# Kernel tuning notes

Hardware: AMD Instinct MI355X
Metric: run time of the kernel (lower is better)

Reference implementation:

```python
import jax, jax.numpy as jnp
import numpy as np

N, G, C, A, E = 10000, 12, 64, 3, 50000
LN_EPS = 1e-5


def setup_inputs() -> dict:
    key = jax.random.key(0)
    ks = jax.random.split(key, 12)
    s = 0.05
    return {
        "x": jax.random.normal(ks[0], (N, G, C), jnp.float32),
        "edge_attr": jax.random.normal(ks[1], (E, G, G, A), jnp.float32),
        "W_kernel": jax.random.normal(ks[2], (A, C), jnp.float32) * s,   # depthwise kernel basis Linear(attr_dim->C)
        "conv_bias": jax.random.normal(ks[3], (C,), jnp.float32) * s,
        "ln_w": jnp.ones((C,), jnp.float32),
        "ln_b": jnp.zeros((C,), jnp.float32),
        "W1": jax.random.normal(ks[4], (C, C), jnp.float32) * s,          # stored [in,out]
        "b1": jax.random.normal(ks[5], (C,), jnp.float32) * s,
        "W2": jax.random.normal(ks[6], (C, C), jnp.float32) * s,
        "b2": jax.random.normal(ks[7], (C,), jnp.float32) * s,
        "layer_scale": jnp.full((1, C), 1e-6, jnp.float32),
        "edge_index": jax.random.randint(ks[8], (2, E), 0, N, jnp.int32),
        "batch": jnp.zeros((N,), jnp.int32),
    }


def reference(x, edge_attr, W_kernel, conv_bias, ln_w, ln_b, W1, b1, W2, b2,
              layer_scale, edge_index, batch):
    src, dst = edge_index[0], edge_index[1]
    x_j = x[src]                                            # [E,G,C] gather
    # depthwise fiber conv: m[e,g,c] = sum_{h,a} attr[e,g,h,a] * Wk[a,c] * x_j[e,h,c]
    # contract over source grid h first to avoid materializing the [E,G,G,C] kernel
    t = jnp.einsum('egha,ehc->egac', edge_attr, x_j)        # [E,G,A,C]
    m = jnp.einsum('egac,ac->egc', t, W_kernel)             # [E,G,C]
    agg = jnp.zeros_like(x).at[dst].add(m) + conv_bias      # scatter-add, [N,G,C]
    # LayerNorm over channel dim
    mu = jnp.mean(agg, axis=-1, keepdims=True)
    var = jnp.mean(jnp.square(agg - mu), axis=-1, keepdims=True)
    h = (agg - mu) * jax.lax.rsqrt(var + LN_EPS) * ln_w + ln_b
    # 2-layer MLP with exact GELU (torch default)
    h = jax.nn.gelu(h @ W1 + b1, approximate=False) @ W2 + b2
    h = layer_scale * h                                     # broadcast [1,C] over [N,G,C]
    return x + h                                            # residual (same shape)
```

## Files before the change

### kernel.cpp

```cpp
#include <hip/hip_runtime.h>
#include <math.h>

#define NN 10000
#define GG 12
#define CC 64
#define AA 3
#define EE 50000
#define LN_EPS 1e-5f
#define MAXDEG 64

typedef __attribute__((ext_vector_type(4))) float f4;
typedef __attribute__((ext_vector_type(4))) short s4;

union S4U { s4 s; unsigned int w[2]; };
union I2S { int i[2]; s4 s; };

__device__ __forceinline__ s4 pack4(float k0, float k1, float k2, float k3) {
    S4U t;
    t.w[0] = __builtin_amdgcn_perm(__float_as_uint(k1), __float_as_uint(k0), 0x07060302u);
    t.w[1] = __builtin_amdgcn_perm(__float_as_uint(k3), __float_as_uint(k2), 0x07060302u);
    return t.s;
}
__device__ __forceinline__ unsigned int pack2(float a, float b) {
    return __builtin_amdgcn_perm(__float_as_uint(b), __float_as_uint(a), 0x07060302u);
}

__device__ __forceinline__ f4 mfma_bf16(s4 a, s4 b, f4 c) {
#if __has_builtin(__builtin_amdgcn_mfma_f32_16x16x16bf16_1k)
    return __builtin_amdgcn_mfma_f32_16x16x16bf16_1k(a, b, c, 0, 0, 0);
#else
    asm volatile("v_mfma_f32_16x16x16_bf16 %0, %1, %2, %0" : "+v"(c) : "v"(a), "v"(b));
    return c;
#endif
}

__global__ __launch_bounds__(256) void xpack(const float* __restrict__ x,
                                             unsigned int* __restrict__ xp,
                                             int* __restrict__ cnt) {
    const int gid = blockIdx.x * 256 + threadIdx.x;
    if (gid < NN) cnt[gid] = 0;

    const int l  = threadIdx.x & 63;
    const int n  = blockIdx.x * 4 + (threadIdx.x >> 6);
    const int lm = l & 15;
    const int lg = l >> 4;

    unsigned int d[8];
    if (lg < 3) {
        const char* xb = (const char*)(x + n * (GG * CC)) + lg * 1024 + lm * 4;
#pragma unroll
        for (int t = 0; t < 4; ++t) {
            const float v0 = *(const float*)(xb + t * 64 + 0 * 256);
            const float v1 = *(const float*)(xb + t * 64 + 1 * 256);
            const float v2 = *(const float*)(xb + t * 64 + 2 * 256);
            const float v3 = *(const float*)(xb + t * 64 + 3 * 256);
            d[2 * t]     = pack2(v0, v1);
            d[2 * t + 1] = pack2(v2, v3);
        }
    } else {
#pragma unroll
        for (int k = 0; k < 8; ++k) d[k] = 0u;
    }
    unsigned int* o = xp + (size_t)n * 512 + l * 8;
    *(uint4*)o       = make_uint4(d[0], d[1], d[2], d[3]);
    *(uint4*)(o + 4) = make_uint4(d[4], d[5], d[6], d[7]);
}

__global__ __launch_bounds__(256) void bucket_fill(const int* __restrict__ ei,
                                                   int* __restrict__ cnt,
                                                   int* __restrict__ elist) {
    int e = blockIdx.x * 256 + threadIdx.x;
    if (e < EE) {
        int src = ei[e];
        int dst = ei[EE + e];
        int pos = atomicAdd(&cnt[dst], 1);
        if (pos < MAXDEG) elist[dst * MAXDEG + pos] = e | (src << 17);
    }
}

__global__ __launch_bounds__(512) void conv_mfma(
    const unsigned int* __restrict__ xp, const float* __restrict__ attr,
    const float* __restrict__ Wk,
    const int* __restrict__ cnt, const int* __restrict__ elist,
    float* __restrict__ agg) {
    __shared__ float lsa[8][2][432];

    const int l  = threadIdx.x & 63;
    const int w  = threadIdx.x >> 6;
    const int lm = l & 15;
    const int lg = l >> 4;

    const int fbase = (lm < 12 && lg < 3) ? (lm * 36 + lg * 12) : 0;
    const int a1l   = (l < 44) ? l : 43;

    float wk[3][4];
#pragma unroll
    for (int a = 0; a < 3; ++a)
#pragma unroll
        for (int t = 0; t < 4; ++t)
            wk[a][t] = Wk[a * CC + lm + 16 * t];

    for (int n = blockIdx.x * 8 + w; n < NN; n += gridDim.x * 8) {
        const int deg = min(cnt[n], MAXDEG);
        const int myE = elist[n * MAXDEG + l];

        f4 acc[3][4];
#pragma unroll
        for (int a = 0; a < 3; ++a)
#pragma unroll
            for (int t = 0; t < 4; ++t) acc[a][t] = (f4){0.f, 0.f, 0.f, 0.f};

        f4 Aa0, Aa1, Ab0, Ab1;
        int4 Xa0, Xa1, Xb0, Xb1;

#define LOADE(idx, A0, A1, X0, X1)                                              \
    {                                                                           \
        const int p = __builtin_amdgcn_readlane(myE, (idx));                    \
        const char* ab = (const char*)(attr + (size_t)(p & 0x1FFFF) * 432);     \
        A0 = *(const f4*)(ab + 16 * l);                                         \
        A1 = *(const f4*)(ab + 1024 + 16 * a1l);                                \
        const int* xb = (const int*)(xp + (size_t)(p >> 17) * 512 + 8 * l);     \
        X0 = *(const int4*)xb;                                                  \
        X1 = *(const int4*)(xb + 4);                                            \
    }

#define STAGE(slot, A0, A1)                                                     \
    {                                                                           \
        float* sw = &lsa[w][slot][0];                                           \
        *(f4*)(sw + 4 * l) = A0;                                                \
        if (l < 44) *(f4*)(sw + 256 + 4 * l) = A1;                              \
    }

#define COMPUTE(slot, X0, X1)                                                   \
    {                                                                           \
        I2S u0, u1, u2, u3;                                                     \
        u0.i[0] = X0.x; u0.i[1] = X0.y;                                         \
        u1.i[0] = X0.z; u1.i[1] = X0.w;                                         \
        u2.i[0] = X1.x; u2.i[1] = X1.y;                                         \
        u3.i[0] = X1.z; u3.i[1] = X1.w;                                         \
        const float* sr = &lsa[w][slot][0] + fbase;                             \
        const f4 q0 = *(const f4*)(sr);                                         \
        const f4 q1 = *(const f4*)(sr + 4);                                     \
        const f4 q2 = *(const f4*)(sr + 8);                                     \
        const s4 af0 = pack4(q0[0], q0[3], q1[2], q2[1]);                       \
        const s4 af1 = pack4(q0[1], q1[0], q1[3], q2[2]);                       \
        const s4 af2 = pack4(q0[2], q1[1], q2[0], q2[3]);                       \
        acc[0][0] = mfma_bf16(af0, u0.s, acc[0][0]);                            \
        acc[1][0] = mfma_bf16(af1, u0.s, acc[1][0]);                            \
        acc[2][0] = mfma_bf16(af2, u0.s, acc[2][0]);                            \
        acc[0][1] = mfma_bf16(af0, u1.s, acc[0][1]);                            \
        acc[1][1] = mfma_bf16(af1, u1.s, acc[1][1]);                            \
        acc[2][1] = mfma_bf16(af2, u1.s, acc[2][1]);                            \
        acc[0][2] = mfma_bf16(af0, u2.s, acc[0][2]);                            \
        acc[1][2] = mfma_bf16(af1, u2.s, acc[1][2]);                            \
        acc[2][2] = mfma_bf16(af2, u2.s, acc[2][2]);                            \
        acc[0][3] = mfma_bf16(af0, u3.s, acc[0][3]);                            \
        acc[1][3] = mfma_bf16(af1, u3.s, acc[1][3]);                            \
        acc[2][3] = mfma_bf16(af2, u3.s, acc[2][3]);                            \
    }

        if (deg > 0) LOADE(0, Aa0, Aa1, Xa0, Xa1);
        if (deg > 1) LOADE(1, Ab0, Ab1, Xb0, Xb1);
        if (deg > 0) STAGE(0, Aa0, Aa1);

        for (int j = 0; j < deg; j += 2) {
            COMPUTE(0, Xa0, Xa1);
            if (j + 2 < deg) LOADE(j + 2, Aa0, Aa1, Xa0, Xa1);
            if (j + 1 < deg) {
                STAGE(1, Ab0, Ab1);
                COMPUTE(1, Xb0, Xb1);
                if (j + 3 < deg) LOADE(j + 3, Ab0, Ab1, Xb0, Xb1);
                if (j + 2 < deg) STAGE(0, Aa0, Aa1);
            }
        }

#undef LOADE
#undef STAGE
#undef COMPUTE

        float* ob = agg + (size_t)n * (GG * CC);
        if (lg < 3) {
#pragma unroll
            for (int t = 0; t < 4; ++t) {
#pragma unroll
                for (int r = 0; r < 4; ++r) {
                    const float m = fmaf(acc[0][t][r], wk[0][t],
                                    fmaf(acc[1][t][r], wk[1][t],
                                         acc[2][t][r] * wk[2][t]));
                    ob[(lg * 4 + r) * CC + lm + 16 * t] = m;
                }
            }
        }
    }
}

__global__ __launch_bounds__(512) void ln_mlp_mfma(
    const float* __restrict__ x, const float* __restrict__ cb,
    const float* __restrict__ lnw, const float* __restrict__ lnb,
    const float* __restrict__ W1, const float* __restrict__ b1,
    const float* __restrict__ W2, const float* __restrict__ b2,
    const float* __restrict__ ls, float* __restrict__ out) {
    __shared__ float sbuf[8][16 * 68];

    const int l  = threadIdx.x & 63;
    const int wv = threadIdx.x >> 6;
    const int lm = l & 15;
    const int lg = l >> 4;
    const int f0 = (blockIdx.x * 8 + wv) * 16;
    if (f0 >= NN * GG) return;

    const float* aggp = out + (size_t)(f0 + lm) * CC + 4 * lg;
    f4 h4[4];
#pragma unroll
    for (int kt = 0; kt < 4; ++kt) h4[kt] = *(const f4*)(aggp + 16 * kt);

    f4 cb4[4], lw4[4], lb4[4];
#pragma unroll
    for (int kt = 0; kt < 4; ++kt) {
        cb4[kt] = *(const f4*)(cb  + 4 * lg + 16 * kt);
        lw4[kt] = *(const f4*)(lnw + 4 * lg + 16 * kt);
        lb4[kt] = *(const f4*)(lnb + 4 * lg + 16 * kt);
    }

    float s = 0.f, s2 = 0.f;
#pragma unroll
    for (int kt = 0; kt < 4; ++kt)
#pragma unroll
        for (int j = 0; j < 4; ++j) {
            const float v = h4[kt][j] + cb4[kt][j];
            h4[kt][j] = v;
            s += v; s2 += v * v;
        }
    s  += __shfl_xor(s, 16);  s  += __shfl_xor(s, 32);
    s2 += __shfl_xor(s2, 16); s2 += __shfl_xor(s2, 32);
    const float mu  = s * (1.f / 64.f);
    const float inv = rsqrtf(s2 * (1.f / 64.f) - mu * mu + LN_EPS);

    s4 hf[4];
#pragma unroll
    for (int kt = 0; kt < 4; ++kt) {
        const float n0 = (h4[kt][0] - mu) * inv * lw4[kt][0] + lb4[kt][0];
        const float n1 = (h4[kt][1] - mu) * inv * lw4[kt][1] + lb4[kt][1];
        const float n2 = (h4[kt][2] - mu) * inv * lw4[kt][2] + lb4[kt][2];
        const float n3 = (h4[kt][3] - mu) * inv * lw4[kt][3] + lb4[kt][3];
        hf[kt] = pack4(n0, n1, n2, n3);
    }

    s4 w1f[4][4];
#pragma unroll
    for (int mt = 0; mt < 4; ++mt)
#pragma unroll
        for (int kt = 0; kt < 4; ++kt) {
            const int kb = 4 * lg + 16 * kt;
            const int m  = lm + 16 * mt;
            w1f[mt][kt] = pack4(W1[(kb + 0) * CC + m], W1[(kb + 1) * CC + m],
                                W1[(kb + 2) * CC + m], W1[(kb + 3) * CC + m]);
        }

    f4 z[4];
#pragma unroll
    for (int mt = 0; mt < 4; ++mt) z[mt] = (f4){0.f, 0.f, 0.f, 0.f};
#pragma unroll
    for (int mt = 0; mt < 4; ++mt)
#pragma unroll
        for (int kt = 0; kt < 4; ++kt)
            z[mt] = mfma_bf16(w1f[mt][kt], hf[kt], z[mt]);

    s4 gf[4];
#pragma unroll
    for (int mt = 0; mt < 4; ++mt) {
        const f4 b14 = *(const f4*)(b1 + 16 * mt + 4 * lg);
        float g[4];
#pragma unroll
        for (int r = 0; r < 4; ++r) {
            const float zz = z[mt][r] + b14[r];
            g[r] = 0.5f * zz * (1.f + erff(zz * 0.70710678118654752f));
        }
        gf[mt] = pack4(g[0], g[1], g[2], g[3]);
    }

    s4 w2f[4][4];
#pragma unroll
    for (int mt = 0; mt < 4; ++mt)
#pragma unroll
        for (int kt = 0; kt < 4; ++kt) {
            const int kb = 4 * lg + 16 * kt;
            const int m  = lm + 16 * mt;
            w2f[mt][kt] = pack4(W2[(kb + 0) * CC + m], W2[(kb + 1) * CC + m],
                                W2[(kb + 2) * CC + m], W2[(kb + 3) * CC + m]);
        }

    f4 o[4];
#pragma unroll
    for (int mt = 0; mt < 4; ++mt) o[mt] = (f4){0.f, 0.f, 0.f, 0.f};
#pragma unroll
    for (int mt = 0; mt < 4; ++mt)
#pragma unroll
        for (int kt = 0; kt < 4; ++kt)
            o[mt] = mfma_bf16(w2f[mt][kt], gf[kt], o[mt]);

    float* sb = sbuf[wv];
    const int fbase = lm * 68;
    const int swz   = (l & 7) << 2;
#pragma unroll
    for (int mt = 0; mt < 4; ++mt)
#pragma unroll
        for (int r = 0; r < 4; ++r)
            sb[fbase + ((16 * mt + 4 * lg + r) ^ swz)] = o[mt][r];

    const f4 b2q = *(const f4*)(b2 + 4 * lm);
    const f4 lsq = *(const f4*)(ls + 4 * lm);

#pragma unroll
    for (int rr = 0; rr < 4; ++rr) {
        const int R   = rr * 4 + lg;
        const int col = 4 * lm;
        const f4 ov = *(const f4*)(&sb[R * 68 + (col ^ ((R & 7) << 2))]);
        const f4 xv = *(const f4*)(x + (size_t)(f0 + R) * CC + col);
        f4 res;
#pragma unroll
        for (int k = 0; k < 4; ++k)
            res[k] = fmaf(lsq[k], ov[k] + b2q[k], xv[k]);
        *(f4*)(out + (size_t)(f0 + R) * CC + col) = res;
    }
}

extern "C" void kernel_launch(void* const* d_in, const int* in_sizes, int n_in,
                              void* d_out, int out_size, void* d_ws, size_t ws_size,
                              hipStream_t stream) {
    const float* x    = (const float*)d_in[0];
    const float* attr = (const float*)d_in[1];
    const float* Wk   = (const float*)d_in[2];
    const float* cb   = (const float*)d_in[3];
    const float* lnw  = (const float*)d_in[4];
    const float* lnb  = (const float*)d_in[5];
    const float* W1   = (const float*)d_in[6];
    const float* b1   = (const float*)d_in[7];
    const float* W2   = (const float*)d_in[8];
    const float* b2   = (const float*)d_in[9];
    const float* ls   = (const float*)d_in[10];
    const int*   ei   = (const int*)d_in[11];
    float* out = (float*)d_out;

    int* cnt   = (int*)d_ws;
    int* elist = cnt + NN;
    unsigned int* xp = (unsigned int*)(elist + NN * MAXDEG);

    xpack<<<NN / 4, 256, 0, stream>>>(x, xp, cnt);
    bucket_fill<<<(EE + 255) / 256, 256, 0, stream>>>(ei, cnt, elist);
    conv_mfma<<<640, 512, 0, stream>>>(xp, attr, Wk, cnt, elist, out);
    ln_mlp_mfma<<<938, 512, 0, stream>>>(x, cb, lnw, lnb, W1, b1, W2, b2, ls, out);
}
```

Measured before the change: 76.63 us.

## Balance conv edge work across waves via per-block shared edge queue

Each block now handles 4 destination nodes and gathers all of their edges into a shared-memory queue. The 4 waves take edges round-robin, so imbalance from uneven node degree within a block is reduced. Each edge's MFMA result is projected by Wk and added atomically into per-node LDS accumulators, then written out together. In exchange it pays for LDS float atomics on every edge, extra block-wide barriers, and a launch of one block per 4 nodes instead of a persistent grid.

```diff
diff --git a/kernel.cpp b/kernel.cpp
--- a/kernel.cpp
+++ b/kernel.cpp
@@ -78,21 +78,47 @@
     }
 }
 
-__global__ __launch_bounds__(512) void conv_mfma(
+__global__ __launch_bounds__(256) void conv_mfma(
     const unsigned int* __restrict__ xp, const float* __restrict__ attr,
     const float* __restrict__ Wk,
     const int* __restrict__ cnt, const int* __restrict__ elist,
     float* __restrict__ agg) {
-    __shared__ float lsa[8][2][432];
+    __shared__ float lsa[4][2][432];
+    __shared__ float nacc[4][GG][68];
+    __shared__ int   qp_[4 * MAXDEG];
+    __shared__ int   qn_[4 * MAXDEG];
+    __shared__ int   degs[4];
 
     const int l  = threadIdx.x & 63;
     const int w  = threadIdx.x >> 6;
+    const int n  = blockIdx.x * 4 + w;
     const int lm = l & 15;
     const int lg = l >> 4;
 
     const int fbase = (lm < 12 && lg < 3) ? (lm * 36 + lg * 12) : 0;
     const int a1l   = (l < 44) ? l : 43;
 
+    const int deg = min(cnt[n], MAXDEG);
+    const int myE = elist[n * MAXDEG + l];
+    if (l == 0) degs[w] = deg;
+
+    {
+        float* nf = &nacc[0][0][0];
+        const f4 z4 = (f4){0.f, 0.f, 0.f, 0.f};
+        for (int q = threadIdx.x; q < 816; q += 256) *(f4*)(nf + q * 4) = z4;
+    }
+    __syncthreads();
+
+    int off = 0, total = 0;
+#pragma unroll
+    for (int j = 0; j < 4; ++j) {
+        const int d = degs[j];
+        if (j < w) off += d;
+        total += d;
+    }
+    if (l < deg) { qp_[off + l] = myE; qn_[off + l] = w; }
+    __syncthreads();
+
     float wk[3][4];
 #pragma unroll
     for (int a = 0; a < 3; ++a)
@@ -100,26 +126,21 @@
         for (int t = 0; t < 4; ++t)
             wk[a][t] = Wk[a * CC + lm + 16 * t];
 
-    for (int n = blockIdx.x * 8 + w; n < NN; n += gridDim.x * 8) {
-        const int deg = min(cnt[n], MAXDEG);
-        const int myE = elist[n * MAXDEG + l];
-
-        f4 acc[3][4];
-#pragma unroll
-        for (int a = 0; a < 3; ++a)
-#pragma unroll
-            for (int t = 0; t < 4; ++t) acc[a][t] = (f4){0.f, 0.f, 0.f, 0.f};
-
-        f4 Aa0, Aa1, Ab0, Ab1;
-        int4 Xa0, Xa1, Xb0, Xb1;
-
-#define LOADE(idx, A0, A1, X0, X1)                                              \
+    const int cntLoc = (total > w) ? ((total - w + 3) >> 2) : 0;
+
+    int Pa = 0, Sa = 0, Pb = 0, Sb = 0;
+    f4 Aa0, Aa1, Ab0, Ab1;
+    int4 Xa0, Xa1, Xb0, Xb1;
+
+#define QLOAD(k, P, S, A0, A1, X0, X1)                                          \
     {                                                                           \
-        const int p = __builtin_amdgcn_readlane(myE, (idx));                    \
-        const char* ab = (const char*)(attr + (size_t)(p & 0x1FFFF) * 432);     \
+        const int qi = w + 4 * (k);                                             \
+        P = __builtin_amdgcn_readfirstlane(qp_[qi]);                            \
+        S = __builtin_amdgcn_readfirstlane(qn_[qi]);                            \
+        const char* ab = (const char*)(attr + (size_t)(P & 0x1FFFF) * 432);     \
         A0 = *(const f4*)(ab + 16 * l);                                         \
         A1 = *(const f4*)(ab + 1024 + 16 * a1l);                                \
-        const int* xb = (const int*)(xp + (size_t)(p >> 17) * 512 + 8 * l);     \
+        const int* xb = (const int*)(xp + (size_t)(P >> 17) * 512 + 8 * l);     \
         X0 = *(const int4*)xb;                                                  \
         X1 = *(const int4*)(xb + 4);                                            \
     }
@@ -131,7 +152,7 @@
         if (l < 44) *(f4*)(sw + 256 + 4 * l) = A1;                              \
     }
 
-#define COMPUTE(slot, X0, X1)                                                   \
+#define COMPUTE(slot, S, X0, X1)                                                \
     {                                                                           \
         I2S u0, u1, u2, u3;                                                     \
         u0.i[0] = X0.x; u0.i[1] = X0.y;                                         \
@@ -145,52 +166,63 @@
         const s4 af0 = pack4(q0[0], q0[3], q1[2], q2[1]);                       \
         const s4 af1 = pack4(q0[1], q1[0], q1[3], q2[2]);                       \
         const s4 af2 = pack4(q0[2], q1[1], q2[0], q2[3]);                       \
-        acc[0][0] = mfma_bf16(af0, u0.s, acc[0][0]);                            \
-        acc[1][0] = mfma_bf16(af1, u0.s, acc[1][0]);                            \
-        acc[2][0] = mfma_bf16(af2, u0.s, acc[2][0]);                            \
-        acc[0][1] = mfma_bf16(af0, u1.s, acc[0][1]);                            \
-        acc[1][1] = mfma_bf16(af1, u1.s, acc[1][1]);                            \
-        acc[2][1] = mfma_bf16(af2, u1.s, acc[2][1]);                            \
-        acc[0][2] = mfma_bf16(af0, u2.s, acc[0][2]);                            \
-        acc[1][2] = mfma_bf16(af1, u2.s, acc[1][2]);                            \
-        acc[2][2] = mfma_bf16(af2, u2.s, acc[2][2]);                            \
-        acc[0][3] = mfma_bf16(af0, u3.s, acc[0][3]);                            \
-        acc[1][3] = mfma_bf16(af1, u3.s, acc[1][3]);                            \
-        acc[2][3] = mfma_bf16(af2, u3.s, acc[2][3]);                            \
-    }
-
-        if (deg > 0) LOADE(0, Aa0, Aa1, Xa0, Xa1);
-        if (deg > 1) LOADE(1, Ab0, Ab1, Xb0, Xb1);
-        if (deg > 0) STAGE(0, Aa0, Aa1);
-
-        for (int j = 0; j < deg; j += 2) {
-            COMPUTE(0, Xa0, Xa1);
-            if (j + 2 < deg) LOADE(j + 2, Aa0, Aa1, Xa0, Xa1);
-            if (j + 1 < deg) {
-                STAGE(1, Ab0, Ab1);
-                COMPUTE(1, Xb0, Xb1);
-                if (j + 3 < deg) LOADE(j + 3, Ab0, Ab1, Xb0, Xb1);
-                if (j + 2 < deg) STAGE(0, Aa0, Aa1);
-            }
-        }
-
-#undef LOADE
+        const f4 z4 = (f4){0.f, 0.f, 0.f, 0.f};                                 \
+        f4 acc[3][4];                                                           \
+        acc[0][0] = mfma_bf16(af0, u0.s, z4);                                   \
+        acc[1][0] = mfma_bf16(af1, u0.s, z4);                                   \
+        acc[2][0] = mfma_bf16(af2, u0.s, z4);                                   \
+        acc[0][1] = mfma_bf16(af0, u1.s, z4);                                   \
+        acc[1][1] = mfma_bf16(af1, u1.s, z4);                                   \
+        acc[2][1] = mfma_bf16(af2, u1.s, z4);                                   \
+        acc[0][2] = mfma_bf16(af0, u2.s, z4);                                   \
+        acc[1][2] = mfma_bf16(af1, u2.s, z4);                                   \
+        acc[2][2] = mfma_bf16(af2, u2.s, z4);                                   \
+        acc[0][3] = mfma_bf16(af0, u3.s, z4);                                   \
+        acc[1][3] = mfma_bf16(af1, u3.s, z4);                                   \
+        acc[2][3] = mfma_bf16(af2, u3.s, z4);                                   \
+        _Pragma("unroll")                                                       \
+        for (int t = 0; t < 4; ++t) {                                           \
+            _Pragma("unroll")                                                   \
+            for (int r = 0; r < 4; ++r) {                                       \
+                const float mv = fmaf(acc[0][t][r], wk[0][t],                   \
+                                 fmaf(acc[1][t][r], wk[1][t],                   \
+                                      acc[2][t][r] * wk[2][t]));                \
+                if (lg < 3)                                                     \
+                    atomicAdd(&nacc[S][lg * 4 + r][lm + 16 * t], mv);           \
+            }                                                                   \
+        }                                                                       \
+    }
+
+    if (cntLoc > 0) QLOAD(0, Pa, Sa, Aa0, Aa1, Xa0, Xa1);
+    if (cntLoc > 1) QLOAD(1, Pb, Sb, Ab0, Ab1, Xb0, Xb1);
+    if (cntLoc > 0) STAGE(0, Aa0, Aa1);
+
+    for (int k = 0; k < cntLoc; k += 2) {
+        COMPUTE(0, Sa, Xa0, Xa1);
+        if (k + 2 < cntLoc) QLOAD(k + 2, Pa, Sa, Aa0, Aa1, Xa0, Xa1);
+        if (k + 1 < cntLoc) {
+            STAGE(1, Ab0, Ab1);
+            COMPUTE(1, Sb, Xb0, Xb1);
+            if (k + 3 < cntLoc) QLOAD(k + 3, Pb, Sb, Ab0, Ab1, Xb0, Xb1);
+            if (k + 2 < cntLoc) STAGE(0, Aa0, Aa1);
+        }
+    }
+
+#undef QLOAD
 #undef STAGE
 #undef COMPUTE
 
-        float* ob = agg + (size_t)n * (GG * CC);
-        if (lg < 3) {
-#pragma unroll
-            for (int t = 0; t < 4; ++t) {
-#pragma unroll
-                for (int r = 0; r < 4; ++r) {
-                    const float m = fmaf(acc[0][t][r], wk[0][t],
-                                    fmaf(acc[1][t][r], wk[1][t],
-                                         acc[2][t][r] * wk[2][t]));
-                    ob[(lg * 4 + r) * CC + lm + 16 * t] = m;
-                }
-            }
-        }
+    __syncthreads();
+
+    float* ob = agg + (size_t)blockIdx.x * 4 * (GG * CC);
+#pragma unroll
+    for (int q = 0; q < 3; ++q) {
+        const int fi  = threadIdx.x + q * 256;
+        const int s   = fi / 192;
+        const int rem = fi % 192;
+        const int g   = rem / 16;
+        const int c4  = (rem % 16) * 4;
+        *(f4*)(ob + fi * 4) = *(const f4*)(&nacc[s][g][c4]);
     }
 }
 
@@ -348,6 +380,6 @@
 
     xpack<<<NN / 4, 256, 0, stream>>>(x, xp, cnt);
     bucket_fill<<<(EE + 255) / 256, 256, 0, stream>>>(ei, cnt, elist);
-    conv_mfma<<<640, 512, 0, stream>>>(xp, attr, Wk, cnt, elist, out);
+    conv_mfma<<<NN / 4, 256, 0, stream>>>(xp, attr, Wk, cnt, elist, out);
     ln_mlp_mfma<<<938, 512, 0, stream>>>(x, cb, lnw, lnb, W1, b1, W2, b2, ls, out);
 }
```

Result: slower. 268.1 us (+249.9%).

## Fuse depthwise conv aggregation with LayerNorm and MLP in one kernel

Applied to the files above, without the earlier changes.

Merges the conv gather-MFMA kernel and the LayerNorm+MLP kernel into one kernel where each wave owns a node and keeps its 12x64 aggregate in LDS instead of writing it to global memory and reading it back. The conv bias is folded in when the aggregate is formed, and the persistent grid-stride loop is replaced by one wave per node with a 4-wave block. This removes one launch and a global round trip of the aggregate, but the MLP now processes only 12 useful rows out of a 16-row MFMA tile (4 padded with zeros), and every wave reloads W1/W2 weights.

```diff
diff --git a/kernel.cpp b/kernel.cpp
--- a/kernel.cpp
+++ b/kernel.cpp
@@ -78,21 +78,29 @@
     }
 }
 
-__global__ __launch_bounds__(512) void conv_mfma(
+__global__ __launch_bounds__(256) void conv_fused(
     const unsigned int* __restrict__ xp, const float* __restrict__ attr,
-    const float* __restrict__ Wk,
-    const int* __restrict__ cnt, const int* __restrict__ elist,
-    float* __restrict__ agg) {
-    __shared__ float lsa[8][2][432];
+    const float* __restrict__ Wk,  const float* __restrict__ cb,
+    const float* __restrict__ lnw, const float* __restrict__ lnb,
+    const float* __restrict__ W1,  const float* __restrict__ b1,
+    const float* __restrict__ W2,  const float* __restrict__ b2,
+    const float* __restrict__ ls,  const float* __restrict__ x,
+    const int* __restrict__ cnt,   const int* __restrict__ elist,
+    float* __restrict__ out) {
+    __shared__ float scratch[4][1088];
 
     const int l  = threadIdx.x & 63;
     const int w  = threadIdx.x >> 6;
+    const int n  = blockIdx.x * 4 + w;
     const int lm = l & 15;
     const int lg = l >> 4;
 
     const int fbase = (lm < 12 && lg < 3) ? (lm * 36 + lg * 12) : 0;
     const int a1l   = (l < 44) ? l : 43;
 
+    const int deg = min(cnt[n], MAXDEG);
+    const int myE = elist[n * MAXDEG + l];
+
     float wk[3][4];
 #pragma unroll
     for (int a = 0; a < 3; ++a)
@@ -100,18 +108,14 @@
         for (int t = 0; t < 4; ++t)
             wk[a][t] = Wk[a * CC + lm + 16 * t];
 
-    for (int n = blockIdx.x * 8 + w; n < NN; n += gridDim.x * 8) {
-        const int deg = min(cnt[n], MAXDEG);
-        const int myE = elist[n * MAXDEG + l];
-
-        f4 acc[3][4];
-#pragma unroll
-        for (int a = 0; a < 3; ++a)
-#pragma unroll
-            for (int t = 0; t < 4; ++t) acc[a][t] = (f4){0.f, 0.f, 0.f, 0.f};
-
-        f4 Aa0, Aa1, Ab0, Ab1;
-        int4 Xa0, Xa1, Xb0, Xb1;
+    f4 acc[3][4];
+#pragma unroll
+    for (int a = 0; a < 3; ++a)
+#pragma unroll
+        for (int t = 0; t < 4; ++t) acc[a][t] = (f4){0.f, 0.f, 0.f, 0.f};
+
+    f4 Aa0, Aa1, Ab0, Ab1;
+    int4 Xa0, Xa1, Xb0, Xb1;
 
 #define LOADE(idx, A0, A1, X0, X1)                                              \
     {                                                                           \
@@ -126,7 +130,7 @@
 
 #define STAGE(slot, A0, A1)                                                     \
     {                                                                           \
-        float* sw = &lsa[w][slot][0];                                           \
+        float* sw = &scratch[w][(slot) * 432];                                  \
         *(f4*)(sw + 4 * l) = A0;                                                \
         if (l < 44) *(f4*)(sw + 256 + 4 * l) = A1;                              \
     }
@@ -138,7 +142,7 @@
         u1.i[0] = X0.z; u1.i[1] = X0.w;                                         \
         u2.i[0] = X1.x; u2.i[1] = X1.y;                                         \
         u3.i[0] = X1.z; u3.i[1] = X1.w;                                         \
-        const float* sr = &lsa[w][slot][0] + fbase;                             \
+        const float* sr = &scratch[w][(slot) * 432] + fbase;                    \
         const f4 q0 = *(const f4*)(sr);                                         \
         const f4 q1 = *(const f4*)(sr + 4);                                     \
         const f4 q2 = *(const f4*)(sr + 8);                                     \
@@ -159,65 +163,50 @@
         acc[2][3] = mfma_bf16(af2, u3.s, acc[2][3]);                            \
     }
 
-        if (deg > 0) LOADE(0, Aa0, Aa1, Xa0, Xa1);
-        if (deg > 1) LOADE(1, Ab0, Ab1, Xb0, Xb1);
-        if (deg > 0) STAGE(0, Aa0, Aa1);
-
-        for (int j = 0; j < deg; j += 2) {
-            COMPUTE(0, Xa0, Xa1);
-            if (j + 2 < deg) LOADE(j + 2, Aa0, Aa1, Xa0, Xa1);
-            if (j + 1 < deg) {
-                STAGE(1, Ab0, Ab1);
-                COMPUTE(1, Xb0, Xb1);
-                if (j + 3 < deg) LOADE(j + 3, Ab0, Ab1, Xb0, Xb1);
-                if (j + 2 < deg) STAGE(0, Aa0, Aa1);
-            }
-        }
+    if (deg > 0) LOADE(0, Aa0, Aa1, Xa0, Xa1);
+    if (deg > 1) LOADE(1, Ab0, Ab1, Xb0, Xb1);
+    if (deg > 0) STAGE(0, Aa0, Aa1);
+
+    for (int j = 0; j < deg; j += 2) {
+        COMPUTE(0, Xa0, Xa1);
+        if (j + 2 < deg) LOADE(j + 2, Aa0, Aa1, Xa0, Xa1);
+        if (j + 1 < deg) {
+            STAGE(1, Ab0, Ab1);
+            COMPUTE(1, Xb0, Xb1);
+            if (j + 3 < deg) LOADE(j + 3, Ab0, Ab1, Xb0, Xb1);
+            if (j + 2 < deg) STAGE(0, Aa0, Aa1);
+        }
+    }
 
 #undef LOADE
 #undef STAGE
 #undef COMPUTE
 
-        float* ob = agg + (size_t)n * (GG * CC);
-        if (lg < 3) {
-#pragma unroll
-            for (int t = 0; t < 4; ++t) {
-#pragma unroll
-                for (int r = 0; r < 4; ++r) {
-                    const float m = fmaf(acc[0][t][r], wk[0][t],
-                                    fmaf(acc[1][t][r], wk[1][t],
-                                         acc[2][t][r] * wk[2][t]));
-                    ob[(lg * 4 + r) * CC + lm + 16 * t] = m;
-                }
+    float* hb = &scratch[w][0];
+
+    if (lg < 3) {
+#pragma unroll
+        for (int t = 0; t < 4; ++t) {
+            const float cbT = cb[lm + 16 * t];
+#pragma unroll
+            for (int r = 0; r < 4; ++r) {
+                const float mv = fmaf(acc[0][t][r], wk[0][t],
+                                 fmaf(acc[1][t][r], wk[1][t],
+                                      acc[2][t][r] * wk[2][t])) + cbT;
+                hb[(4 * lg + r) * 68 + lm + 16 * t] = mv;
             }
         }
     }
-}
-
-__global__ __launch_bounds__(512) void ln_mlp_mfma(
-    const float* __restrict__ x, const float* __restrict__ cb,
-    const float* __restrict__ lnw, const float* __restrict__ lnb,
-    const float* __restrict__ W1, const float* __restrict__ b1,
-    const float* __restrict__ W2, const float* __restrict__ b2,
-    const float* __restrict__ ls, float* __restrict__ out) {
-    __shared__ float sbuf[8][16 * 68];
-
-    const int l  = threadIdx.x & 63;
-    const int wv = threadIdx.x >> 6;
-    const int lm = l & 15;
-    const int lg = l >> 4;
-    const int f0 = (blockIdx.x * 8 + wv) * 16;
-    if (f0 >= NN * GG) return;
-
-    const float* aggp = out + (size_t)(f0 + lm) * CC + 4 * lg;
+    *(f4*)(hb + (12 + lg) * 68 + 4 * lm) = (f4){0.f, 0.f, 0.f, 0.f};
+
     f4 h4[4];
 #pragma unroll
-    for (int kt = 0; kt < 4; ++kt) h4[kt] = *(const f4*)(aggp + 16 * kt);
-
-    f4 cb4[4], lw4[4], lb4[4];
+    for (int kt = 0; kt < 4; ++kt)
+        h4[kt] = *(const f4*)(hb + lm * 68 + 4 * lg + 16 * kt);
+
+    f4 lw4[4], lb4[4];
 #pragma unroll
     for (int kt = 0; kt < 4; ++kt) {
-        cb4[kt] = *(const f4*)(cb  + 4 * lg + 16 * kt);
         lw4[kt] = *(const f4*)(lnw + 4 * lg + 16 * kt);
         lb4[kt] = *(const f4*)(lnb + 4 * lg + 16 * kt);
     }
@@ -227,8 +216,7 @@
     for (int kt = 0; kt < 4; ++kt)
 #pragma unroll
         for (int j = 0; j < 4; ++j) {
-            const float v = h4[kt][j] + cb4[kt][j];
-            h4[kt][j] = v;
+            const float v = h4[kt][j];
             s += v; s2 += v * v;
         }
     s  += __shfl_xor(s, 16);  s  += __shfl_xor(s, 32);
@@ -246,25 +234,19 @@
         hf[kt] = pack4(n0, n1, n2, n3);
     }
 
-    s4 w1f[4][4];
+    f4 z[4];
+#pragma unroll
+    for (int mt = 0; mt < 4; ++mt) z[mt] = (f4){0.f, 0.f, 0.f, 0.f};
 #pragma unroll
     for (int mt = 0; mt < 4; ++mt)
 #pragma unroll
         for (int kt = 0; kt < 4; ++kt) {
             const int kb = 4 * lg + 16 * kt;
             const int m  = lm + 16 * mt;
-            w1f[mt][kt] = pack4(W1[(kb + 0) * CC + m], W1[(kb + 1) * CC + m],
+            const s4 wf = pack4(W1[(kb + 0) * CC + m], W1[(kb + 1) * CC + m],
                                 W1[(kb + 2) * CC + m], W1[(kb + 3) * CC + m]);
-        }
-
-    f4 z[4];
-#pragma unroll
-    for (int mt = 0; mt < 4; ++mt) z[mt] = (f4){0.f, 0.f, 0.f, 0.f};
-#pragma unroll
-    for (int mt = 0; mt < 4; ++mt)
-#pragma unroll
-        for (int kt = 0; kt < 4; ++kt)
-            z[mt] = mfma_bf16(w1f[mt][kt], hf[kt], z[mt]);
+            z[mt] = mfma_bf16(wf, hf[kt], z[mt]);
+        }
 
     s4 gf[4];
 #pragma unroll
@@ -279,43 +261,37 @@
         gf[mt] = pack4(g[0], g[1], g[2], g[3]);
     }
 
-    s4 w2f[4][4];
+    f4 o[4];
+#pragma unroll
+    for (int mt = 0; mt < 4; ++mt) o[mt] = (f4){0.f, 0.f, 0.f, 0.f};
 #pragma unroll
     for (int mt = 0; mt < 4; ++mt)
 #pragma unroll
         for (int kt = 0; kt < 4; ++kt) {
             const int kb = 4 * lg + 16 * kt;
             const int m  = lm + 16 * mt;
-            w2f[mt][kt] = pack4(W2[(kb + 0) * CC + m], W2[(kb + 1) * CC + m],
+            const s4 wf = pack4(W2[(kb + 0) * CC + m], W2[(kb + 1) * CC + m],
                                 W2[(kb + 2) * CC + m], W2[(kb + 3) * CC + m]);
-        }
-
-    f4 o[4];
-#pragma unroll
-    for (int mt = 0; mt < 4; ++mt) o[mt] = (f4){0.f, 0.f, 0.f, 0.f};
+            o[mt] = mfma_bf16(wf, gf[kt], o[mt]);
+        }
+
+    const int fb2 = lm * 68;
+    const int swz = (l & 7) << 2;
 #pragma unroll
     for (int mt = 0; mt < 4; ++mt)
 #pragma unroll
-        for (int kt = 0; kt < 4; ++kt)
-            o[mt] = mfma_bf16(w2f[mt][kt], gf[kt], o[mt]);
-
-    float* sb = sbuf[wv];
-    const int fbase = lm * 68;
-    const int swz   = (l & 7) << 2;
-#pragma unroll
-    for (int mt = 0; mt < 4; ++mt)
-#pragma unroll
         for (int r = 0; r < 4; ++r)
-            sb[fbase + ((16 * mt + 4 * lg + r) ^ swz)] = o[mt][r];
+            hb[fb2 + ((16 * mt + 4 * lg + r) ^ swz)] = o[mt][r];
 
     const f4 b2q = *(const f4*)(b2 + 4 * lm);
     const f4 lsq = *(const f4*)(ls + 4 * lm);
-
-#pragma unroll
-    for (int rr = 0; rr < 4; ++rr) {
+    const int f0 = n * GG;
+
+#pragma unroll
+    for (int rr = 0; rr < 3; ++rr) {
         const int R   = rr * 4 + lg;
         const int col = 4 * lm;
-        const f4 ov = *(const f4*)(&sb[R * 68 + (col ^ ((R & 7) << 2))]);
+        const f4 ov = *(const f4*)(&hb[R * 68 + (col ^ ((R & 7) << 2))]);
         const f4 xv = *(const f4*)(x + (size_t)(f0 + R) * CC + col);
         f4 res;
 #pragma unroll
@@ -348,6 +324,6 @@
 
     xpack<<<NN / 4, 256, 0, stream>>>(x, xp, cnt);
     bucket_fill<<<(EE + 255) / 256, 256, 0, stream>>>(ei, cnt, elist);
-    conv_mfma<<<640, 512, 0, stream>>>(xp, attr, Wk, cnt, elist, out);
-    ln_mlp_mfma<<<938, 512, 0, stream>>>(x, cb, lnw, lnb, W1, b1, W2, b2, ls, out);
-}
+    conv_fused<<<NN / 4, 256, 0, stream>>>(xp, attr, Wk, cb, lnw, lnb, W1, b1,
+                                           W2, b2, ls, x, cnt, elist, out);
+}
```

Result: faster. 69.61 us (-9.2%).
